# Optimization experiments

Hardware: AMD Instinct MI355X
Metric: run time of the kernel (lower is better)

Reference implementation:

```python
import jax, jax.numpy as jnp
import numpy as np

B, N, D, OUT = 1024, 64, 512, 2048


def setup_inputs() -> dict:
    key = jax.random.key(0)
    k1, k2, k3, k4 = jax.random.split(key, 4)
    semantic_vec = jax.random.normal(k1, (B, D), dtype=jnp.float32)
    vertices = jax.random.normal(k2, (N, D), dtype=jnp.float32)
    # per-branch Linear weights/biases, stacked: W[n] is [OUT, D], b[n] is [OUT]
    scale = 1.0 / np.sqrt(D)
    W = jax.random.uniform(k3, (N, OUT, D), dtype=jnp.float32, minval=-scale, maxval=scale)
    b = jax.random.uniform(k4, (N, OUT), dtype=jnp.float32, minval=-scale, maxval=scale)
    return {"semantic_vec": semantic_vec, "vertices": vertices, "W": W, "b": b}


def reference(semantic_vec, vertices, W, b):
    # offsets: [B, N, D] = semantic_vec broadcast-minus each vertice
    offsets = semantic_vec[:, None, :] - vertices[None, :, :]
    # per-branch linear: [B, N, OUT]
    resp = jnp.einsum('bnd,nod->bno', offsets, W) + b[None, :, :]
    resp = jax.nn.relu(resp)
    # sum over the N branches -> [B, OUT]
    return resp.sum(axis=1)
```

## Files before the change

### kernel.cpp

```cpp
#include <hip/hip_runtime.h>
#include <hip/hip_bf16.h>


typedef __attribute__((ext_vector_type(8)))  short bf16x8;
typedef __attribute__((ext_vector_type(4)))  short bf16x4;
typedef __attribute__((ext_vector_type(4)))  float f32x4;
typedef __attribute__((ext_vector_type(16))) float f32x16;

constexpr int B   = 1024;
constexpr int N   = 64;
constexpr int D   = 512;
constexpr int OUT = 2048;

constexpr int BM  = 128;
constexpr int BO  = 64;
constexpr int TPB = 512;

static __device__ __forceinline__ unsigned short f2bf(float f) {
    unsigned int u = __builtin_bit_cast(unsigned int, f);
    u += 0x7FFFu + ((u >> 16) & 1u);
    return (unsigned short)(u >> 16);
}

static __device__ __forceinline__ bf16x4 cvt4(float4 a) {
    bf16x4 r;
    r[0] = (short)f2bf(a.x); r[1] = (short)f2bf(a.y);
    r[2] = (short)f2bf(a.z); r[3] = (short)f2bf(a.w);
    return r;
}

static __device__ __forceinline__ bf16x8 cvt8(float4 a, float4 b) {
    bf16x8 r;
    r[0] = (short)f2bf(a.x); r[1] = (short)f2bf(a.y);
    r[2] = (short)f2bf(a.z); r[3] = (short)f2bf(a.w);
    r[4] = (short)f2bf(b.x); r[5] = (short)f2bf(b.y);
    r[6] = (short)f2bf(b.z); r[7] = (short)f2bf(b.w);
    return r;
}

__global__ __launch_bounds__(256) void prep_kernel(const float* __restrict__ W,
                                                   const float* __restrict__ V,
                                                   const float* __restrict__ bias,
                                                   unsigned short* __restrict__ Wb,
                                                   float* __restrict__ c) {
    const int wid  = (blockIdx.x * 256 + threadIdx.x) >> 6;
    const int lane = threadIdx.x & 63;
    const int n = wid >> 11;

    const size_t rbase = (size_t)wid * D;
    float4 w0 = *reinterpret_cast<const float4*>(W + rbase + lane * 4);
    float4 w1 = *reinterpret_cast<const float4*>(W + rbase + 256 + lane * 4);
    float4 v0 = *reinterpret_cast<const float4*>(V + (size_t)n * D + lane * 4);
    float4 v1 = *reinterpret_cast<const float4*>(V + (size_t)n * D + 256 + lane * 4);

    *reinterpret_cast<bf16x4*>(Wb + rbase + lane * 4)       = cvt4(w0);
    *reinterpret_cast<bf16x4*>(Wb + rbase + 256 + lane * 4) = cvt4(w1);

    float s = w0.x * v0.x + w0.y * v0.y + w0.z * v0.z + w0.w * v0.w
            + w1.x * v1.x + w1.y * v1.y + w1.z * v1.z + w1.w * v1.w;
    #pragma unroll
    for (int off = 1; off < 64; off <<= 1) s += __shfl_xor(s, off);
    if (lane == 0) c[wid] = bias[wid] - s;
}

__global__ __launch_bounds__(TPB) void main_kernel(const float* __restrict__ S,
                                                   const unsigned short* __restrict__ Wb,
                                                   const float* __restrict__ C,
                                                   float* __restrict__ out) {
    __shared__ unsigned short As[BM * D];

    const int t    = threadIdx.x;
    const int lane = t & 63;
    const int w    = t >> 6;
    const int og   = w & 1;
    const int ng   = w >> 1;
    const int oc   = lane & 31;
    const int hi   = lane >> 5;
    const int ob0  = blockIdx.x * BO;
    const int bm0  = blockIdx.y * BM;
    const int ocol = ob0 + og * 32 + oc;

    #pragma unroll
    for (int i = 0; i < (BM * D / 8) / TPB; ++i) {
        int cid = i * TPB + t;
        int row = cid >> 6;
        int kc  = cid & 63;
        const float4* sp = reinterpret_cast<const float4*>(S + (size_t)(bm0 + row) * D + kc * 8);
        bf16x8 val = cvt8(sp[0], sp[1]);
        *reinterpret_cast<bf16x8*>(&As[row * D + ((kc ^ (row & 15)) * 8)]) = val;
    }
    __syncthreads();

    f32x16 oacc[4];
    #pragma unroll
    for (int mi = 0; mi < 4; ++mi)
        #pragma unroll
        for (int r = 0; r < 16; ++r) oacc[mi][r] = 0.f;

    for (int nc = 0; nc < 8; ++nc) {
        const int n0 = ng * 16 + nc * 2;

        f32x16 pre[2][4];
        #pragma unroll
        for (int j = 0; j < 2; ++j)
            #pragma unroll
            for (int mi = 0; mi < 4; ++mi)
                #pragma unroll
                for (int r = 0; r < 16; ++r) pre[j][mi][r] = 0.f;

        const unsigned short* wb0 = Wb + ((size_t)n0 * OUT + ocol) * D + hi * 8;
        const unsigned short* wb1 = wb0 + (size_t)OUT * D;

        #pragma unroll 4
        for (int ks = 0; ks < 32; ++ks) {
            bf16x8 bq0 = *reinterpret_cast<const bf16x8*>(wb0 + ks * 16);
            bf16x8 bq1 = *reinterpret_cast<const bf16x8*>(wb1 + ks * 16);
            const int kc2 = ks * 2 + hi;
            #pragma unroll
            for (int mi = 0; mi < 4; ++mi) {
                const int row = mi * 32 + oc;
                bf16x8 aq = *reinterpret_cast<const bf16x8*>(
                    &As[row * D + ((kc2 ^ (row & 15)) * 8)]);
                pre[0][mi] = __builtin_amdgcn_mfma_f32_32x32x16_bf16(aq, bq0, pre[0][mi], 0, 0, 0);
                pre[1][mi] = __builtin_amdgcn_mfma_f32_32x32x16_bf16(aq, bq1, pre[1][mi], 0, 0, 0);
            }
        }

        #pragma unroll
        for (int j = 0; j < 2; ++j) {
            const float cv = C[(n0 + j) * OUT + ocol];
            #pragma unroll
            for (int mi = 0; mi < 4; ++mi)
                #pragma unroll
                for (int r = 0; r < 16; ++r)
                    oacc[mi][r] += fmaxf(pre[j][mi][r] + cv, 0.f);
        }
    }

    __syncthreads();
    float* red = reinterpret_cast<float*>(As);
    if (ng != 0) {
        const int slab = ((ng - 1) * 2 + og) * 4096;
        #pragma unroll
        for (int mi = 0; mi < 4; ++mi) {
            #pragma unroll
            for (int rg = 0; rg < 4; ++rg) {
                f32x4 v = {oacc[mi][rg * 4 + 0], oacc[mi][rg * 4 + 1],
                           oacc[mi][rg * 4 + 2], oacc[mi][rg * 4 + 3]};
                *reinterpret_cast<f32x4*>(&red[slab + (mi * 4 + rg) * 256 + lane * 4]) = v;
            }
        }
    }
    __syncthreads();
    if (ng == 0) {
        #pragma unroll
        for (int mi = 0; mi < 4; ++mi) {
            #pragma unroll
            for (int rg = 0; rg < 4; ++rg) {
                f32x4 sum = {oacc[mi][rg * 4 + 0], oacc[mi][rg * 4 + 1],
                             oacc[mi][rg * 4 + 2], oacc[mi][rg * 4 + 3]};
                #pragma unroll
                for (int s = 0; s < 3; ++s) {
                    const int slab = (s * 2 + og) * 4096;
                    f32x4 o2 = *reinterpret_cast<const f32x4*>(
                        &red[slab + (mi * 4 + rg) * 256 + lane * 4]);
                    #pragma unroll
                    for (int q = 0; q < 4; ++q) sum[q] += o2[q];
                }
                #pragma unroll
                for (int q = 0; q < 4; ++q) {
                    const int row = bm0 + mi * 32 + q + 8 * rg + 4 * hi;
                    out[(size_t)row * OUT + ocol] = sum[q];
                }
            }
        }
    }
}

__global__ __launch_bounds__(512) void fused_kernel(const float* __restrict__ S,
                                                    const float* __restrict__ W,
                                                    const float* __restrict__ V,
                                                    const float* __restrict__ bias,
                                                    float* __restrict__ out) {
    __shared__ unsigned short As3[128 * D];

    const int t    = threadIdx.x;
    const int lane = t & 63;
    const int w    = t >> 6;
    const int og   = w & 3;
    const int ngh  = w >> 2;
    const int l15  = lane & 15;
    const int lg   = lane >> 4;
    const int ob0  = blockIdx.x * 64;
    const int bm0  = blockIdx.y * 128;
    const int ocol = ob0 + og * 16 + l15;

    #pragma unroll
    for (int i = 0; i < (128 * D / 8) / 512; ++i) {
        int cid = i * 512 + t;
        int row = cid >> 6;
        int kc  = cid & 63;
        const float4* sp = reinterpret_cast<const float4*>(S + (size_t)(bm0 + row) * D + kc * 8);
        bf16x8 val = cvt8(sp[0], sp[1]);
        *reinterpret_cast<bf16x8*>(&As3[row * D + ((kc ^ (row & 7)) * 8)]) = val;
    }
    __syncthreads();

    f32x4 oacc[8];
    #pragma unroll
    for (int mi = 0; mi < 8; ++mi) oacc[mi] = (f32x4){0.f, 0.f, 0.f, 0.f};

    const int kofs = lg * 8;

    for (int nc = 0; nc < 8; ++nc) {
        const int n0 = ngh * 32 + nc * 4;

        f32x4 pre[4][8];
        #pragma unroll
        for (int j = 0; j < 4; ++j)
            #pragma unroll
            for (int mi = 0; mi < 8; ++mi) pre[j][mi] = (f32x4){0.f, 0.f, 0.f, 0.f};

        float cacc[4] = {0.f, 0.f, 0.f, 0.f};

        const float* wbase = W + ((size_t)n0 * OUT + ocol) * D + kofs;
        const float* vbase = V + (size_t)n0 * D + kofs;

        #pragma unroll 2
        for (int ks = 0; ks < 16; ++ks) {
            bf16x8 bq[4];
            #pragma unroll
            for (int j = 0; j < 4; ++j) {
                const float* wr = wbase + (size_t)j * (OUT * D) + ks * 32;
                float4 wa = *reinterpret_cast<const float4*>(wr);
                float4 wb = *reinterpret_cast<const float4*>(wr + 4);
                const float* vr = vbase + (size_t)j * D + ks * 32;
                float4 va = *reinterpret_cast<const float4*>(vr);
                float4 vb = *reinterpret_cast<const float4*>(vr + 4);
                cacc[j] += wa.x * va.x + wa.y * va.y + wa.z * va.z + wa.w * va.w
                         + wb.x * vb.x + wb.y * vb.y + wb.z * vb.z + wb.w * vb.w;
                bq[j] = cvt8(wa, wb);
            }
            const int kc = ks * 4 + lg;
            #pragma unroll
            for (int mi = 0; mi < 8; ++mi) {
                const int row = mi * 16 + l15;
                bf16x8 aq = *reinterpret_cast<const bf16x8*>(
                    &As3[row * D + ((kc ^ (row & 7)) * 8)]);
                pre[0][mi] = __builtin_amdgcn_mfma_f32_16x16x32_bf16(aq, bq[0], pre[0][mi], 0, 0, 0);
                pre[1][mi] = __builtin_amdgcn_mfma_f32_16x16x32_bf16(aq, bq[1], pre[1][mi], 0, 0, 0);
                pre[2][mi] = __builtin_amdgcn_mfma_f32_16x16x32_bf16(aq, bq[2], pre[2][mi], 0, 0, 0);
                pre[3][mi] = __builtin_amdgcn_mfma_f32_16x16x32_bf16(aq, bq[3], pre[3][mi], 0, 0, 0);
            }
        }

        #pragma unroll
        for (int j = 0; j < 4; ++j) {
            float cs = cacc[j];
            cs += __shfl_xor(cs, 16);
            cs += __shfl_xor(cs, 32);
            const float cv = bias[(n0 + j) * OUT + ocol] - cs;
            #pragma unroll
            for (int mi = 0; mi < 8; ++mi)
                #pragma unroll
                for (int r = 0; r < 4; ++r)
                    oacc[mi][r] += fmaxf(pre[j][mi][r] + cv, 0.f);
        }
    }

    __syncthreads();
    float* red = reinterpret_cast<float*>(As3);
    if (ngh == 1) {
        #pragma unroll
        for (int mi = 0; mi < 8; ++mi)
            *reinterpret_cast<f32x4*>(&red[(og * 8 + mi) * 256 + lane * 4]) = oacc[mi];
    }
    __syncthreads();
    if (ngh == 0) {
        #pragma unroll
        for (int mi = 0; mi < 8; ++mi) {
            f32x4 o2 = *reinterpret_cast<const f32x4*>(&red[(og * 8 + mi) * 256 + lane * 4]);
            #pragma unroll
            for (int r = 0; r < 4; ++r) {
                int row = bm0 + mi * 16 + lg * 4 + r;
                out[(size_t)row * OUT + ocol] = oacc[mi][r] + o2[r];
            }
        }
    }
}

extern "C" void kernel_launch(void* const* d_in, const int* in_sizes, int n_in,
                              void* d_out, int out_size, void* d_ws, size_t ws_size,
                              hipStream_t stream) {
    const float* S    = (const float*)d_in[0];
    const float* V    = (const float*)d_in[1];
    const float* W    = (const float*)d_in[2];
    const float* bias = (const float*)d_in[3];
    float* out = (float*)d_out;

    const size_t wb_bytes = (size_t)N * OUT * D * sizeof(unsigned short);
    const size_t c_bytes  = (size_t)N * OUT * sizeof(float);

    if (ws_size >= wb_bytes + c_bytes) {
        unsigned short* Wb = (unsigned short*)d_ws;
        float*          c  = (float*)((char*)d_ws + wb_bytes);
        prep_kernel<<<dim3((N * OUT) / 4), dim3(256), 0, stream>>>(W, V, bias, Wb, c);
        main_kernel<<<dim3(OUT / BO, B / BM), dim3(TPB), 0, stream>>>(S, Wb, c, out);
    } else {
        fused_kernel<<<dim3(OUT / 64, B / 128), dim3(512), 0, stream>>>(S, W, V, bias, out);
    }
}
```

Before: 215.0 us.

## Pre-swizzle bf16 weights into MFMA fragment order for coalesced B loads

The prep kernel now stages each 64x512 weight tile in LDS and writes it back in the exact per-lane MFMA fragment order, so each wavefront's B-operand load in the main kernel is one contiguous 1KB read instead of strided 16-byte reads across rows. The bias-correction dot product is now computed from the bf16-rounded weights by 64 threads per block. This trades a heavier prep pass (LDS staging, a serial dot loop on one wave) for better coalescing of the dominant weight stream. The correction term now uses bf16 weights, which slightly changes numerics.

```diff
diff --git a/kernel.cpp b/kernel.cpp
--- a/kernel.cpp
+++ b/kernel.cpp
@@ -3,7 +3,6 @@
 
 
 typedef __attribute__((ext_vector_type(8)))  short bf16x8;
-typedef __attribute__((ext_vector_type(4)))  short bf16x4;
 typedef __attribute__((ext_vector_type(4)))  float f32x4;
 typedef __attribute__((ext_vector_type(16))) float f32x16;
 
@@ -22,11 +21,9 @@
     return (unsigned short)(u >> 16);
 }
 
-static __device__ __forceinline__ bf16x4 cvt4(float4 a) {
-    bf16x4 r;
-    r[0] = (short)f2bf(a.x); r[1] = (short)f2bf(a.y);
-    r[2] = (short)f2bf(a.z); r[3] = (short)f2bf(a.w);
-    return r;
+static __device__ __forceinline__ float bf2f(unsigned short u) {
+    unsigned int x = ((unsigned int)u) << 16;
+    return __builtin_bit_cast(float, x);
 }
 
 static __device__ __forceinline__ bf16x8 cvt8(float4 a, float4 b) {
@@ -41,30 +38,60 @@
 __global__ __launch_bounds__(256) void prep_kernel(const float* __restrict__ W,
                                                    const float* __restrict__ V,
                                                    const float* __restrict__ bias,
-                                                   unsigned short* __restrict__ Wb,
+                                                   unsigned short* __restrict__ Wswz,
                                                    float* __restrict__ c) {
-    const int wid  = (blockIdx.x * 256 + threadIdx.x) >> 6;
-    const int lane = threadIdx.x & 63;
-    const int n = wid >> 11;
-
-    const size_t rbase = (size_t)wid * D;
-    float4 w0 = *reinterpret_cast<const float4*>(W + rbase + lane * 4);
-    float4 w1 = *reinterpret_cast<const float4*>(W + rbase + 256 + lane * 4);
-    float4 v0 = *reinterpret_cast<const float4*>(V + (size_t)n * D + lane * 4);
-    float4 v1 = *reinterpret_cast<const float4*>(V + (size_t)n * D + 256 + lane * 4);
-
-    *reinterpret_cast<bf16x4*>(Wb + rbase + lane * 4)       = cvt4(w0);
-    *reinterpret_cast<bf16x4*>(Wb + rbase + 256 + lane * 4) = cvt4(w1);
-
-    float s = w0.x * v0.x + w0.y * v0.y + w0.z * v0.z + w0.w * v0.w
-            + w1.x * v1.x + w1.y * v1.y + w1.z * v1.z + w1.w * v1.w;
-    #pragma unroll
-    for (int off = 1; off < 64; off <<= 1) s += __shfl_xor(s, off);
-    if (lane == 0) c[wid] = bias[wid] - s;
+    __shared__ unsigned short L[64 * 512];
+
+    const int nb = blockIdx.x;
+    const int n  = nb >> 5;
+    const int ob = nb & 31;
+    const int t  = threadIdx.x;
+
+    #pragma unroll
+    for (int i = 0; i < 16; ++i) {
+        const int cid = i * 256 + t;
+        const int r   = cid >> 6;
+        const int kc  = cid & 63;
+        const float4* wp = reinterpret_cast<const float4*>(
+            W + ((size_t)n * OUT + ob * 64 + r) * D + kc * 8);
+        bf16x8 v8 = cvt8(wp[0], wp[1]);
+        *reinterpret_cast<bf16x8*>(&L[r * 512 + ((kc ^ (r & 15)) * 8)]) = v8;
+    }
+    __syncthreads();
+
+    if (t < 64) {
+        const int r = t;
+        float s = 0.f;
+        #pragma unroll 8
+        for (int kc = 0; kc < 64; ++kc) {
+            bf16x8 wv = *reinterpret_cast<const bf16x8*>(&L[r * 512 + ((kc ^ (r & 15)) * 8)]);
+            const float4 va = *reinterpret_cast<const float4*>(V + (size_t)n * D + kc * 8);
+            const float4 vb = *reinterpret_cast<const float4*>(V + (size_t)n * D + kc * 8 + 4);
+            s += bf2f((unsigned short)wv[0]) * va.x + bf2f((unsigned short)wv[1]) * va.y
+               + bf2f((unsigned short)wv[2]) * va.z + bf2f((unsigned short)wv[3]) * va.w
+               + bf2f((unsigned short)wv[4]) * vb.x + bf2f((unsigned short)wv[5]) * vb.y
+               + bf2f((unsigned short)wv[6]) * vb.z + bf2f((unsigned short)wv[7]) * vb.w;
+        }
+        const int o = ob * 64 + r;
+        c[n * OUT + o] = bias[n * OUT + o] - s;
+    }
+
+    const size_t obase = ((size_t)(n * 32 + ob) * 64) * 512;
+    #pragma unroll
+    for (int i = 0; i < 16; ++i) {
+        const int cid  = i * 256 + t;
+        const int lane = cid & 63;
+        const int og   = (cid >> 6) & 1;
+        const int ks   = cid >> 7;
+        const int row  = og * 32 + (lane & 31);
+        const int kc   = ks * 2 + (lane >> 5);
+        bf16x8 v8 = *reinterpret_cast<const bf16x8*>(&L[row * 512 + ((kc ^ (row & 15)) * 8)]);
+        *reinterpret_cast<bf16x8*>(&Wswz[obase + (size_t)(cid >> 6) * 512 + lane * 8]) = v8;
+    }
 }
 
 __global__ __launch_bounds__(TPB) void main_kernel(const float* __restrict__ S,
-                                                   const unsigned short* __restrict__ Wb,
+                                                   const unsigned short* __restrict__ Wswz,
                                                    const float* __restrict__ C,
                                                    float* __restrict__ out) {
     __shared__ unsigned short As[BM * D];
@@ -76,9 +103,9 @@
     const int ng   = w >> 1;
     const int oc   = lane & 31;
     const int hi   = lane >> 5;
-    const int ob0  = blockIdx.x * BO;
+    const int ob   = blockIdx.x;
     const int bm0  = blockIdx.y * BM;
-    const int ocol = ob0 + og * 32 + oc;
+    const int ocol = ob * BO + og * 32 + oc;
 
     #pragma unroll
     for (int i = 0; i < (BM * D / 8) / TPB; ++i) {
@@ -108,13 +135,14 @@
                 #pragma unroll
                 for (int r = 0; r < 16; ++r) pre[j][mi][r] = 0.f;
 
-        const unsigned short* wb0 = Wb + ((size_t)n0 * OUT + ocol) * D + hi * 8;
-        const unsigned short* wb1 = wb0 + (size_t)OUT * D;
+        const unsigned short* wb0 =
+            Wswz + ((size_t)(n0 * 32 + ob) * 64 + og) * 512 + lane * 8;
+        const unsigned short* wb1 = wb0 + (size_t)2048 * 512;
 
         #pragma unroll 4
         for (int ks = 0; ks < 32; ++ks) {
-            bf16x8 bq0 = *reinterpret_cast<const bf16x8*>(wb0 + ks * 16);
-            bf16x8 bq1 = *reinterpret_cast<const bf16x8*>(wb1 + ks * 16);
+            bf16x8 bq0 = *reinterpret_cast<const bf16x8*>(wb0 + ks * 1024);
+            bf16x8 bq1 = *reinterpret_cast<const bf16x8*>(wb1 + ks * 1024);
             const int kc2 = ks * 2 + hi;
             #pragma unroll
             for (int mi = 0; mi < 4; ++mi) {
@@ -302,10 +330,10 @@
     const size_t c_bytes  = (size_t)N * OUT * sizeof(float);
 
     if (ws_size >= wb_bytes + c_bytes) {
-        unsigned short* Wb = (unsigned short*)d_ws;
-        float*          c  = (float*)((char*)d_ws + wb_bytes);
-        prep_kernel<<<dim3((N * OUT) / 4), dim3(256), 0, stream>>>(W, V, bias, Wb, c);
-        main_kernel<<<dim3(OUT / BO, B / BM), dim3(TPB), 0, stream>>>(S, Wb, c, out);
+        unsigned short* Wswz = (unsigned short*)d_ws;
+        float*          c    = (float*)((char*)d_ws + wb_bytes);
+        prep_kernel<<<dim3(N * 32), dim3(256), 0, stream>>>(W, V, bias, Wswz, c);
+        main_kernel<<<dim3(OUT / BO, B / BM), dim3(TPB), 0, stream>>>(S, Wswz, c, out);
     } else {
         fused_kernel<<<dim3(OUT / 64, B / 128), dim3(512), 0, stream>>>(S, W, V, bias, out);
     }
```

Result: slower. 249.9 us (+16.2%).
